# Kernel optimization log

Measured on AMD Instinct MI355X. Metric: run time of the kernel, lower is better.

## Reference

```python
import jax, jax.numpy as jnp
import numpy as np

N_NODES = 30000
N_REL = 8
N_EDGES = 150000
EMB = 128
HID = 128
OUT = 256
HEADS = 4
RANK = 8
SCALE = 1.0
NEG_SLOPE = 0.2
LN_EPS = 1e-5


def setup_inputs():
    key = jax.random.key(0)
    ks = jax.random.split(key, 16)
    def nrm(k, shp, s=0.05):
        return jax.random.normal(k, shp, dtype=jnp.float32) * s
    d2 = HEADS * HID  # conv2 input dim = 512
    return {
        "entity_emb": nrm(ks[0], (N_NODES, EMB)),
        "A1": nrm(ks[1], (N_REL, EMB * RANK)),
        "B1": nrm(ks[2], (N_REL, EMB * RANK)),
        "W1": nrm(ks[3], (HEADS * HID, EMB)),
        "att_l1": nrm(ks[4], (1, HEADS, HID)),
        "att_r1": nrm(ks[5], (1, HEADS, HID)),
        "relb1": jnp.zeros((N_REL, HEADS), jnp.float32),
        "bias1": jnp.zeros((HEADS * HID,), jnp.float32),
        "A2": nrm(ks[6], (N_REL, d2 * RANK)),
        "B2": nrm(ks[7], (N_REL, d2 * RANK)),
        "W2": nrm(ks[8], (OUT, d2)),
        "att_l2": nrm(ks[9], (1, 1, OUT)),
        "att_r2": nrm(ks[10], (1, 1, OUT)),
        "relb2": jnp.zeros((N_REL, 1), jnp.float32),
        "bias2": jnp.zeros((OUT,), jnp.float32),
        "res_W": nrm(ks[11], (OUT, EMB)),
        "res_b": jnp.zeros((OUT,), jnp.float32),
        "ln_g": jnp.ones((OUT,), jnp.float32),
        "ln_b": jnp.zeros((OUT,), jnp.float32),
        "edge_index": jax.random.randint(ks[12], (2, N_EDGES), 0, N_NODES),
        "edge_type": jax.random.randint(ks[13], (N_EDGES,), 0, N_REL),
    }


def _rel_gat_conv(x, A, B, W, att_l, att_r, relb, bias, j_idx, i_idx, etype, heads, out_dim, concat):
    # x: [N,d]; A,B: [R, d*k]; W: [heads*out_dim, d]
    N, d = x.shape
    R = A.shape[0]
    k = RANK
    HC = heads * out_dim
    A3 = A.reshape(R, d, k)
    B3 = B.reshape(R, d, k)
    z_all = x @ W.T  # [N, HC] base linear (shared by z_i and z_j)
    # LoRA low-rank projection per (node, relation): P[n,r] = B_r^T x_n
    P = jnp.einsum('nd,rdk->nrk', x, B3)          # [N,R,k] (small)
    low = P[j_idx, etype]                          # [E,k]
    # Fused LoRA-through-lin: lin(scale*A_r B_r^T x) = scale * low @ (A_r^T W^T)
    M = jnp.einsum('rdk,hd->rkh', A3, W).reshape(R * k, HC)  # [R*k, HC]
    oh = jax.nn.one_hot(etype, R, dtype=x.dtype)   # [E,R]
    low_exp = (oh[:, :, None] * low[:, None, :]).reshape(-1, R * k)  # [E,R*k]
    z_j = (z_all[j_idx] + SCALE * (low_exp @ M)).reshape(-1, heads, out_dim)  # [E,H,C]
    z_i = z_all[i_idx].reshape(-1, heads, out_dim)                            # [E,H,C]
    alpha = (z_i * att_l).sum(-1) + (z_j * att_r).sum(-1) + relb[etype]       # [E,H]
    alpha = jax.nn.leaky_relu(alpha, NEG_SLOPE)
    # per-relation loop => softmax groups are (relation, target node)
    seg = etype * N + i_idx
    n_seg = R * N
    amax = jax.ops.segment_max(alpha, seg, num_segments=n_seg)
    ex = jnp.exp(alpha - amax[seg])
    den = jax.ops.segment_sum(ex, seg, num_segments=n_seg)
    alpha = ex / den[seg]
    msg = z_j * alpha[:, :, None]                  # [E,H,C]
    out = jax.ops.segment_sum(msg, i_idx, num_segments=N)  # [N,H,C]
    out = out.reshape(N, HC) if concat else out.mean(axis=1)
    return out + bias


def _forward(entity_emb, A1, B1, W1, att_l1, att_r1, relb1, bias1,
             A2, B2, W2, att_l2, att_r2, relb2, bias2,
             res_W, res_b, ln_g, ln_b, edge_index, edge_type):
    j_idx, i_idx = edge_index[0], edge_index[1]
    x0 = entity_emb
    x = _rel_gat_conv(x0, A1, B1, W1, att_l1, att_r1, relb1, bias1,
                      j_idx, i_idx, edge_type, HEADS, HID, True)
    x = jax.nn.elu(x)
    x = _rel_gat_conv(x, A2, B2, W2, att_l2, att_r2, relb2, bias2,
                      j_idx, i_idx, edge_type, 1, OUT, False)
    x = x + (x0 @ res_W.T + res_b)
    mu = x.mean(axis=-1, keepdims=True)
    var = ((x - mu) ** 2).mean(axis=-1, keepdims=True)
    return (x - mu) / jnp.sqrt(var + LN_EPS) * ln_g + ln_b


def reference(entity_emb, A1, B1, W1, att_l1, att_r1, relb1, bias1,
              A2, B2, W2, att_l2, att_r2, relb2, bias2,
              res_W, res_b, ln_g, ln_b, edge_index, edge_type):
    return _forward(entity_emb, A1, B1, W1, att_l1, att_r1, relb1, bias1,
                    A2, B2, W2, att_l2, att_r2, relb2, bias2,
                    res_W, res_b, ln_g, ln_b, edge_index, edge_type)
```

## Files before the change

### kernel.cpp

```cpp
#include <hip/hip_runtime.h>
#include <cstddef>

#define NRELS 8
#define EMB 128
#define HID 128
#define OUTD 256
#define HEADS 4
#define RANK 8
#define D2 512
#define KCAT 192
#define NEG_SLOPE 0.2f
#define LN_EPS 1e-5f

typedef short bf16x8 __attribute__((ext_vector_type(8)));
typedef float f32x4 __attribute__((ext_vector_type(4)));

__device__ __forceinline__ unsigned short f2bf(float f) {
  union { float f; unsigned u; } v; v.f = f;
  unsigned u = v.u;
  return (unsigned short)((u + 0x7fffu + ((u >> 16) & 1u)) >> 16);
}
__device__ __forceinline__ float bf2f(unsigned short u) {
  union { unsigned u; float f; } v; v.u = (unsigned)u << 16; return v.f;
}

template<int ATT, int BIAS>
__global__ __launch_bounds__(256) void gemm_big_h(const unsigned short* __restrict__ A,
    const unsigned short* __restrict__ B, unsigned short* __restrict__ C, int M, int N, int K,
    const float* __restrict__ bias, const float* __restrict__ attL,
    const float* __restrict__ attR, float* __restrict__ al, float* __restrict__ ar) {
  __shared__ unsigned short As[128][36];
  __shared__ unsigned short Bs[128][36];
  __shared__ float pL[2][128];
  __shared__ float pR[2][128];
  const int tid = threadIdx.x;
  const int wave = tid >> 6;
  const int lane = tid & 63;
  const int wm = wave & 1;
  const int wn = wave >> 1;
  const int r16 = lane & 15;
  const int quad = lane >> 4;
  const int bm = blockIdx.x * 128;
  const int bn = blockIdx.y * 128;
  const int srow = tid >> 2;
  const int scol = (tid & 3) * 8;
  int ar0 = bm + srow;      if (ar0 >= M) ar0 = M - 1;
  int ar1 = bm + 64 + srow; if (ar1 >= M) ar1 = M - 1;
  const unsigned short* Ag0 = A + (size_t)ar0 * K + scol;
  const unsigned short* Ag1 = A + (size_t)ar1 * K + scol;
  const unsigned short* Bg0 = B + (size_t)(bn + srow) * K + scol;
  const unsigned short* Bg1 = B + (size_t)(bn + 64 + srow) * K + scol;
  f32x4 acc[4][4] = {};
  for (int k0 = 0; k0 < K; k0 += 32) {
    bf16x8 a0 = *(const bf16x8*)(Ag0 + k0);
    bf16x8 a1 = *(const bf16x8*)(Ag1 + k0);
    bf16x8 b0 = *(const bf16x8*)(Bg0 + k0);
    bf16x8 b1 = *(const bf16x8*)(Bg1 + k0);
    __syncthreads();
    *(bf16x8*)(&As[srow][scol]) = a0;
    *(bf16x8*)(&As[64 + srow][scol]) = a1;
    *(bf16x8*)(&Bs[srow][scol]) = b0;
    *(bf16x8*)(&Bs[64 + srow][scol]) = b1;
    __syncthreads();
    bf16x8 af[4], bfr[4];
#pragma unroll
    for (int mi = 0; mi < 4; ++mi)
      af[mi] = *(const bf16x8*)(&As[wm * 64 + mi * 16 + r16][quad * 8]);
#pragma unroll
    for (int ni = 0; ni < 4; ++ni)
      bfr[ni] = *(const bf16x8*)(&Bs[wn * 64 + ni * 16 + r16][quad * 8]);
#pragma unroll
    for (int mi = 0; mi < 4; ++mi)
#pragma unroll
      for (int ni = 0; ni < 4; ++ni)
        acc[mi][ni] = __builtin_amdgcn_mfma_f32_16x16x32_bf16(af[mi], bfr[ni], acc[mi][ni], 0, 0, 0);
  }
  float bcol[4];
  if (BIAS) {
#pragma unroll
    for (int ni = 0; ni < 4; ++ni) bcol[ni] = bias[bn + wn * 64 + ni * 16 + r16];
  }
#pragma unroll
  for (int mi = 0; mi < 4; ++mi)
#pragma unroll
    for (int ni = 0; ni < 4; ++ni)
#pragma unroll
      for (int r = 0; r < 4; ++r) {
        int row = bm + wm * 64 + mi * 16 + quad * 4 + r;
        if (row < M) {
          float v = acc[mi][ni][r];
          if (BIAS) v += bcol[ni];
          C[(size_t)row * N + bn + wn * 64 + ni * 16 + r16] = f2bf(v);
        }
      }
  if (ATT) {
    float La[4], Ra[4];
#pragma unroll
    for (int ni = 0; ni < 4; ++ni) {
      int cn = bn + wn * 64 + ni * 16 + r16;
      La[ni] = attL[cn]; Ra[ni] = attR[cn];
    }
#pragma unroll
    for (int mi = 0; mi < 4; ++mi)
#pragma unroll
      for (int r = 0; r < 4; ++r) {
        float sl = 0.f, sr = 0.f;
#pragma unroll
        for (int ni = 0; ni < 4; ++ni) {
          sl = fmaf(acc[mi][ni][r], La[ni], sl);
          sr = fmaf(acc[mi][ni][r], Ra[ni], sr);
        }
#pragma unroll
        for (int o = 1; o < 16; o <<= 1) {
          sl += __shfl_xor(sl, o, 64);
          sr += __shfl_xor(sr, o, 64);
        }
        if (r16 == 0) {
          int rl = wm * 64 + mi * 16 + quad * 4 + r;
          pL[wn][rl] = sl; pR[wn][rl] = sr;
        }
      }
    __syncthreads();
    if (tid < 128) {
      int row = bm + tid;
      if (row < M) {
        float sl = pL[0][tid] + pL[1][tid];
        float sr = pR[0][tid] + pR[1][tid];
        if (ATT == 1) {
          al[(size_t)row * 4 + blockIdx.y] = sl;
          ar[(size_t)row * 4 + blockIdx.y] = sr;
        } else {
          atomicAdd(&al[row], sl);
          atomicAdd(&ar[row], sr);
        }
      }
    }
  }
}

__global__ __launch_bounds__(256) void gemm_big(const unsigned short* __restrict__ A,
    const unsigned short* __restrict__ B, float* __restrict__ C, int M, int N, int K,
    const float* __restrict__ b0p, const float* __restrict__ b1p) {
  __shared__ unsigned short As[128][36];
  __shared__ unsigned short Bs[128][36];
  const int tid = threadIdx.x;
  const int wave = tid >> 6;
  const int lane = tid & 63;
  const int wm = wave & 1;
  const int wn = wave >> 1;
  const int r16 = lane & 15;
  const int quad = lane >> 4;
  const int bm = blockIdx.x * 128;
  const int bn = blockIdx.y * 128;
  const int srow = tid >> 2;
  const int scol = (tid & 3) * 8;
  int ar0 = bm + srow;      if (ar0 >= M) ar0 = M - 1;
  int ar1 = bm + 64 + srow; if (ar1 >= M) ar1 = M - 1;
  const unsigned short* Ag0 = A + (size_t)ar0 * K + scol;
  const unsigned short* Ag1 = A + (size_t)ar1 * K + scol;
  const unsigned short* Bg0 = B + (size_t)(bn + srow) * K + scol;
  const unsigned short* Bg1 = B + (size_t)(bn + 64 + srow) * K + scol;
  f32x4 acc[4][4] = {};
  for (int k0 = 0; k0 < K; k0 += 32) {
    bf16x8 a0 = *(const bf16x8*)(Ag0 + k0);
    bf16x8 a1 = *(const bf16x8*)(Ag1 + k0);
    bf16x8 b0 = *(const bf16x8*)(Bg0 + k0);
    bf16x8 b1 = *(const bf16x8*)(Bg1 + k0);
    __syncthreads();
    *(bf16x8*)(&As[srow][scol]) = a0;
    *(bf16x8*)(&As[64 + srow][scol]) = a1;
    *(bf16x8*)(&Bs[srow][scol]) = b0;
    *(bf16x8*)(&Bs[64 + srow][scol]) = b1;
    __syncthreads();
    bf16x8 af[4], bfr[4];
#pragma unroll
    for (int mi = 0; mi < 4; ++mi)
      af[mi] = *(const bf16x8*)(&As[wm * 64 + mi * 16 + r16][quad * 8]);
#pragma unroll
    for (int ni = 0; ni < 4; ++ni)
      bfr[ni] = *(const bf16x8*)(&Bs[wn * 64 + ni * 16 + r16][quad * 8]);
#pragma unroll
    for (int mi = 0; mi < 4; ++mi)
#pragma unroll
      for (int ni = 0; ni < 4; ++ni)
        acc[mi][ni] = __builtin_amdgcn_mfma_f32_16x16x32_bf16(af[mi], bfr[ni], acc[mi][ni], 0, 0, 0);
  }
  float badd[4];
#pragma unroll
  for (int ni = 0; ni < 4; ++ni) {
    int cn = bn + wn * 64 + ni * 16 + r16;
    badd[ni] = b0p[cn] + b1p[cn];
  }
#pragma unroll
  for (int mi = 0; mi < 4; ++mi)
#pragma unroll
    for (int ni = 0; ni < 4; ++ni)
#pragma unroll
      for (int r = 0; r < 4; ++r) {
        int row = bm + wm * 64 + mi * 16 + quad * 4 + r;
        if (row < M)
          C[(size_t)row * N + bn + wn * 64 + ni * 16 + r16] = acc[mi][ni][r] + badd[ni];
      }
}

__global__ __launch_bounds__(256) void gemm_bf16t(const unsigned short* __restrict__ A,
    const unsigned short* __restrict__ B, float* __restrict__ C, int M, int N, int K) {
  __shared__ unsigned short As[64][40];
  __shared__ unsigned short Bs[64][40];
  const int tid = threadIdx.x;
  const int wave = tid >> 6;
  const int lane = tid & 63;
  const int wm = wave & 1;
  const int wn = wave >> 1;
  const int r16 = lane & 15;
  const int quad = lane >> 4;
  const int bm = blockIdx.x * 64;
  const int bn = blockIdx.y * 64;
  const int srow = tid >> 2;
  const int schunk = tid & 3;
  int arow = bm + srow; if (arow >= M) arow = M - 1;
  const unsigned short* Ag = A + (size_t)arow * K + schunk * 8;
  const unsigned short* Bg = B + (size_t)(bn + srow) * K + schunk * 8;
  f32x4 acc[2][2] = {};
  for (int k0 = 0; k0 < K; k0 += 32) {
    bf16x8 av = *(const bf16x8*)(Ag + k0);
    bf16x8 bv = *(const bf16x8*)(Bg + k0);
    __syncthreads();
    *(bf16x8*)(&As[srow][schunk * 8]) = av;
    *(bf16x8*)(&Bs[srow][schunk * 8]) = bv;
    __syncthreads();
    bf16x8 af0 = *(const bf16x8*)(&As[wm * 32 + r16][quad * 8]);
    bf16x8 af1 = *(const bf16x8*)(&As[wm * 32 + 16 + r16][quad * 8]);
    bf16x8 bf0 = *(const bf16x8*)(&Bs[wn * 32 + r16][quad * 8]);
    bf16x8 bf1 = *(const bf16x8*)(&Bs[wn * 32 + 16 + r16][quad * 8]);
    acc[0][0] = __builtin_amdgcn_mfma_f32_16x16x32_bf16(af0, bf0, acc[0][0], 0, 0, 0);
    acc[0][1] = __builtin_amdgcn_mfma_f32_16x16x32_bf16(af0, bf1, acc[0][1], 0, 0, 0);
    acc[1][0] = __builtin_amdgcn_mfma_f32_16x16x32_bf16(af1, bf0, acc[1][0], 0, 0, 0);
    acc[1][1] = __builtin_amdgcn_mfma_f32_16x16x32_bf16(af1, bf1, acc[1][1], 0, 0, 0);
  }
#pragma unroll
  for (int mi = 0; mi < 2; ++mi)
#pragma unroll
    for (int ni = 0; ni < 2; ++ni)
#pragma unroll
      for (int r = 0; r < 4; ++r) {
        int row = bm + wm * 32 + mi * 16 + quad * 4 + r;
        if (row < M)
          C[(size_t)row * N + bn + wn * 32 + ni * 16 + r16] = acc[mi][ni][r];
      }
}

__global__ __launch_bounds__(256) void gemm_abt(const float* __restrict__ A,
    const float* __restrict__ B, float* __restrict__ C, int M, int N, int K) {
  __shared__ float As[32][64];
  __shared__ float Bs[32][64];
  const int tid = threadIdx.x;
  const int bm = blockIdx.y * 64;
  const int bn = blockIdx.x * 64;
  const int tx = tid & 15;
  const int ty = tid >> 4;
  const int lr = tid & 63;
  const int lq = tid >> 6;
  float acc[4][4] = {};
  for (int k0 = 0; k0 < K; k0 += 32) {
#pragma unroll
    for (int s = 0; s < 2; ++s) {
      const int q = lq + s * 4;
      const int gm = bm + lr;
      float4 va = make_float4(0.f, 0.f, 0.f, 0.f);
      if (gm < M) va = *(const float4*)(A + (size_t)gm * K + k0 + q * 4);
      As[q * 4 + 0][lr] = va.x; As[q * 4 + 1][lr] = va.y;
      As[q * 4 + 2][lr] = va.z; As[q * 4 + 3][lr] = va.w;
      const int gn = bn + lr;
      float4 vb = *(const float4*)(B + (size_t)gn * K + k0 + q * 4);
      Bs[q * 4 + 0][lr] = vb.x; Bs[q * 4 + 1][lr] = vb.y;
      Bs[q * 4 + 2][lr] = vb.z; Bs[q * 4 + 3][lr] = vb.w;
    }
    __syncthreads();
#pragma unroll
    for (int kk = 0; kk < 32; ++kk) {
      float a[4], b[4];
#pragma unroll
      for (int i2 = 0; i2 < 4; ++i2) { a[i2] = As[kk][ty * 4 + i2]; b[i2] = Bs[kk][tx * 4 + i2]; }
#pragma unroll
      for (int i2 = 0; i2 < 4; ++i2)
#pragma unroll
        for (int j2 = 0; j2 < 4; ++j2)
          acc[i2][j2] = fmaf(a[i2], b[j2], acc[i2][j2]);
    }
    __syncthreads();
  }
#pragma unroll
  for (int i2 = 0; i2 < 4; ++i2) {
    const int gm = bm + ty * 4 + i2;
    if (gm >= M) continue;
#pragma unroll
    for (int j2 = 0; j2 < 4; ++j2)
      C[(size_t)gm * N + bn + tx * 4 + j2] = acc[i2][j2];
  }
}

__global__ void prep_all(const float* __restrict__ x0, const float* __restrict__ W1,
    const float* __restrict__ W2, const float* __restrict__ res_W,
    const float* __restrict__ A1, const float* __restrict__ A2,
    const float* __restrict__ B1, const float* __restrict__ B2,
    unsigned short* __restrict__ x0b, unsigned short* __restrict__ Acat,
    unsigned short* __restrict__ W1b, unsigned short* __restrict__ W2b,
    unsigned short* __restrict__ RWcat,
    float* __restrict__ Amat1, float* __restrict__ Amat2,
    unsigned short* __restrict__ Bmat1b, unsigned short* __restrict__ Bmat2b, int nx0) {
  int idx = blockIdx.x * 256 + threadIdx.x;
  if (idx < nx0) { unsigned short b = f2bf(x0[idx]); x0b[idx] = b;
    Acat[(size_t)(idx >> 7) * KCAT + (idx & 127)] = b; return; } idx -= nx0;
  if (idx < D2 * EMB) { W1b[idx] = f2bf(W1[idx]); return; } idx -= D2 * EMB;
  if (idx < OUTD * D2) { W2b[idx] = f2bf(W2[idx]); return; } idx -= OUTD * D2;
  if (idx < OUTD * EMB) { RWcat[(size_t)(idx >> 7) * KCAT + (idx & 127)] = f2bf(res_W[idx]); return; } idx -= OUTD * EMB;
  if (idx < 64 * EMB) { int d = idx % EMB, rk = idx / EMB, k = rk & 7, r = rk >> 3;
    Amat1[idx] = A1[(size_t)r * EMB * RANK + (size_t)d * RANK + k]; return; } idx -= 64 * EMB;
  if (idx < 64 * D2) { int d = idx % D2, rk = idx / D2, k = rk & 7, r = rk >> 3;
    Amat2[idx] = A2[(size_t)r * D2 * RANK + (size_t)d * RANK + k]; return; } idx -= 64 * D2;
  if (idx < 64 * EMB) { int d = idx % EMB, rk = idx / EMB, k = rk & 7, r = rk >> 3;
    Bmat1b[idx] = f2bf(B1[(size_t)r * EMB * RANK + (size_t)d * RANK + k]); return; } idx -= 64 * EMB;
  if (idx < 64 * D2) { int d = idx % D2, rk = idx / D2, k = rk & 7, r = rk >> 3;
    Bmat2b[idx] = f2bf(B2[(size_t)r * D2 * RANK + (size_t)d * RANK + k]); }
}

__global__ void fold_att(const float* __restrict__ M1, const float* __restrict__ attR1,
                         const float* __restrict__ M2, const float* __restrict__ attR2,
                         float* __restrict__ Matt1, float* __restrict__ Matt2) {
  int t = threadIdx.x;
  if (blockIdx.x == 0) {
    int h = t & 3, rk = t >> 2;
    float s = 0.f;
    for (int c = 0; c < HID; ++c)
      s = fmaf(M1[(size_t)rk * D2 + h * HID + c], attR1[h * HID + c], s);
    Matt1[rk * 4 + h] = s;
  } else if (t < 64) {
    float s = 0.f;
    for (int c = 0; c < OUTD; ++c) s = fmaf(M2[(size_t)t * OUTD + c], attR2[c], s);
    Matt2[t] = s;
  }
}

__global__ void build_MT(const float* __restrict__ M1, const float* __restrict__ M2,
                         unsigned short* __restrict__ M1T, unsigned short* __restrict__ RWcat) {
  int idx = blockIdx.x * 256 + threadIdx.x;
  if (idx < 512 * 256) {
    int c = idx >> 8, s = idx & 255;
    int h = s >> 6, rk = s & 63;
    float v = ((c >> 7) == h) ? M1[(size_t)rk * D2 + c] : 0.f;
    M1T[idx] = f2bf(v);
  } else {
    idx -= 512 * 256;
    if (idx < 256 * 64) {
      int c = idx >> 6, rk = idx & 63;
      RWcat[(size_t)c * KCAT + 128 + rk] = f2bf(M2[(size_t)rk * OUTD + c]);
    }
  }
}

__global__ void hist_kernel(const int* __restrict__ ii, int* __restrict__ deg, int E) {
  int e = blockIdx.x * blockDim.x + threadIdx.x;
  if (e < E) atomicAdd(&deg[ii[e]], 1);
}

__global__ __launch_bounds__(1024) void exscan_kernel(const int* __restrict__ deg,
                                                      int* __restrict__ rowstart, int n) {
  __shared__ int wsum[16];
  int t = threadIdx.x;
  int lane = t & 63, wid = t >> 6;
  int carry = 0;
  for (int base = 0; base < n; base += 4096) {
    int i0 = base + t * 4;
    int v0 = 0, v1 = 0, v2 = 0, v3 = 0;
    if (i0 + 3 < n) {
      int4 vv = *(const int4*)(deg + i0);
      v0 = vv.x; v1 = vv.y; v2 = vv.z; v3 = vv.w;
    } else {
      if (i0 < n) v0 = deg[i0];
      if (i0 + 1 < n) v1 = deg[i0 + 1];
      if (i0 + 2 < n) v2 = deg[i0 + 2];
      if (i0 + 3 < n) v3 = deg[i0 + 3];
    }
    int tot = v0 + v1 + v2 + v3;
    int x = tot;
#pragma unroll
    for (int o = 1; o < 64; o <<= 1) {
      int y = __shfl_up(x, o, 64);
      if (lane >= o) x += y;
    }
    if (lane == 63) wsum[wid] = x;
    __syncthreads();
    if (t == 0) {
      int s = carry;
      for (int w2 = 0; w2 < 16; ++w2) { int tmp = wsum[w2]; wsum[w2] = s; s += tmp; }
      carry = s;
    }
    __syncthreads();
    int ex0 = x - tot + wsum[wid];
    if (i0 + 3 < n) {
      int4 ov; ov.x = ex0; ov.y = ex0 + v0; ov.z = ex0 + v0 + v1; ov.w = ex0 + v0 + v1 + v2;
      *(int4*)(rowstart + i0) = ov;
    } else {
      if (i0 < n) rowstart[i0] = ex0;
      if (i0 + 1 < n) rowstart[i0 + 1] = ex0 + v0;
      if (i0 + 2 < n) rowstart[i0 + 2] = ex0 + v0 + v1;
      if (i0 + 3 < n) rowstart[i0 + 3] = ex0 + v0 + v1 + v2;
    }
    __syncthreads();
  }
  if (t == 0) rowstart[n] = carry;
}

__global__ void scatter_kernel(const int* __restrict__ ii, const int* __restrict__ rowstart,
                               int* __restrict__ cursor, int* __restrict__ slot_of, int E) {
  int e = blockIdx.x * blockDim.x + threadIdx.x;
  if (e >= E) return;
  int i = ii[e];
  int p = atomicAdd(&cursor[i], 1);
  slot_of[e] = rowstart[i] + p;
}

__global__ void edge_alpha1(const int* __restrict__ ji, const int* __restrict__ ii,
                            const int* __restrict__ et, const int* __restrict__ slot_of,
                            const float* __restrict__ P1,
                            const float* __restrict__ al1, const float* __restrict__ ar1,
                            const float* __restrict__ relb1, const float* __restrict__ Matt1,
                            float4* __restrict__ recs1, int E) {
  int e = blockIdx.x * blockDim.x + threadIdx.x;
  if (e >= E) return;
  int j = ji[e], i = ii[e], rt = et[e];
  float4 lo0 = *(const float4*)(P1 + (size_t)j * 64 + rt * 8);
  float4 lo1 = *(const float4*)(P1 + (size_t)j * 64 + rt * 8 + 4);
  float low[RANK] = {lo0.x, lo0.y, lo0.z, lo0.w, lo1.x, lo1.y, lo1.z, lo1.w};
  float4 ali = *(const float4*)(al1 + (size_t)i * 4);
  float4 arj = *(const float4*)(ar1 + (size_t)j * 4);
  float4 rb  = *(const float4*)(relb1 + rt * 4);
  float a0 = ali.x + arj.x + rb.x;
  float a1 = ali.y + arj.y + rb.y;
  float a2 = ali.z + arj.z + rb.z;
  float a3 = ali.w + arj.w + rb.w;
#pragma unroll
  for (int k = 0; k < RANK; ++k) {
    float4 mk = *(const float4*)(Matt1 + ((rt * 8 + k) << 2));
    a0 = fmaf(low[k], mk.x, a0); a1 = fmaf(low[k], mk.y, a1);
    a2 = fmaf(low[k], mk.z, a2); a3 = fmaf(low[k], mk.w, a3);
  }
  a0 = (a0 > 0.f) ? a0 : NEG_SLOPE * a0;
  a1 = (a1 > 0.f) ? a1 : NEG_SLOPE * a1;
  a2 = (a2 > 0.f) ? a2 : NEG_SLOPE * a2;
  a3 = (a3 > 0.f) ? a3 : NEG_SLOPE * a3;
  float e0 = expf(a0), e1 = expf(a1), e2 = expf(a2), e3 = expf(a3);
  float4* rp = recs1 + (size_t)slot_of[e] * 4;
  rp[0] = make_float4(__int_as_float(j), e0, e1, e2);
  rp[1] = make_float4(e3, __int_as_float(rt), low[0], low[1]);
  rp[2] = make_float4(low[2], low[3], low[4], low[5]);
  rp[3] = make_float4(low[6], low[7], 0.f, 0.f);
}

__global__ __launch_bounds__(256) void qden1(float4* __restrict__ recs1,
    const int* __restrict__ rowstart, unsigned short* __restrict__ Q1b, int Nn) {
  __shared__ float denS[4][32];
  const int wid = threadIdx.x >> 6, lane = threadIdx.x & 63;
  const int i = blockIdx.x * 4 + wid;
  if (i >= Nn) return;
  const int rt_mine = lane >> 3, k = lane & 7;
  const int s0 = rowstart[i], deg = rowstart[i + 1] - s0;
  const float* rf = (const float*)recs1;
  float q0 = 0.f, q1 = 0.f, q2 = 0.f, q3 = 0.f;
  float d0 = 0.f, d1 = 0.f, d2 = 0.f, d3 = 0.f;
  float4 a0 = {}, a1 = {};
  float lw = 0.f;
  if (deg > 0) {
    a0 = recs1[(size_t)s0 * 4]; a1 = recs1[(size_t)s0 * 4 + 1];
    lw = rf[(size_t)s0 * 16 + 6 + k];
  }
  for (int p = 0; p < deg; ++p) {
    float4 b0 = a0, b1 = a1; float lwn = lw;
    if (p + 1 < deg) {
      b0 = recs1[(size_t)(s0 + p + 1) * 4]; b1 = recs1[(size_t)(s0 + p + 1) * 4 + 1];
      lwn = rf[(size_t)(s0 + p + 1) * 16 + 6 + k];
    }
    int rt = __float_as_int(a1.y);
    if (rt == rt_mine) {
      q0 = fmaf(a0.y, lw, q0); q1 = fmaf(a0.z, lw, q1);
      q2 = fmaf(a0.w, lw, q2); q3 = fmaf(a1.x, lw, q3);
      d0 += a0.y; d1 += a0.z; d2 += a0.w; d3 += a1.x;
    }
    a0 = b0; a1 = b1; lw = lwn;
  }
  float r0 = (d0 > 0.f) ? 1.f / d0 : 0.f;
  float r1 = (d1 > 0.f) ? 1.f / d1 : 0.f;
  float r2 = (d2 > 0.f) ? 1.f / d2 : 0.f;
  float r3 = (d3 > 0.f) ? 1.f / d3 : 0.f;
  size_t qb = (size_t)i * 256;
  Q1b[qb + lane]       = f2bf(q0 * r0);
  Q1b[qb + 64 + lane]  = f2bf(q1 * r1);
  Q1b[qb + 128 + lane] = f2bf(q2 * r2);
  Q1b[qb + 192 + lane] = f2bf(q3 * r3);
  if (k == 0) {
    denS[wid][rt_mine]      = r0;
    denS[wid][8 + rt_mine]  = r1;
    denS[wid][16 + rt_mine] = r2;
    denS[wid][24 + rt_mine] = r3;
  }
  for (int p = lane; p < deg; p += 64) {
    float4* rp = recs1 + (size_t)(s0 + p) * 4;
    float4 v0 = rp[0]; float4 v1 = rp[1];
    int rt = __float_as_int(v1.y);
    v0.y *= denS[wid][rt];      v0.z *= denS[wid][8 + rt];
    v0.w *= denS[wid][16 + rt]; v1.x *= denS[wid][24 + rt];
    rp[0] = v0; rp[1] = v1;
  }
}

__global__ __launch_bounds__(256) void node_agg1_lite(const float4* __restrict__ recs1,
    const int* __restrict__ rowstart, const unsigned short* __restrict__ z1b,
    const unsigned short* __restrict__ L1b, unsigned short* __restrict__ h1out, int Nn) {
  const int wid = threadIdx.x >> 6;
  const int lane = threadIdx.x & 63;
  const int i = blockIdx.x * 4 + wid;
  if (i >= Nn) return;
  const int s0 = rowstart[i];
  const int deg = rowstart[i + 1] - s0;
  const int c0 = lane * 8;
  const float* rf = (const float*)recs1;
  float acc[8] = {};
  float4 rc = {}, rn = {};
  float w3c = 0.f, w3n = 0.f;
  uint4 zc = {};
  if (deg > 0) {
    rc = recs1[(size_t)s0 * 4];
    w3c = rf[(size_t)s0 * 16 + 4];
    zc = *(const uint4*)(z1b + (size_t)__float_as_int(rc.x) * D2 + c0);
  }
  if (deg > 1) {
    rn = recs1[(size_t)(s0 + 1) * 4];
    w3n = rf[(size_t)(s0 + 1) * 16 + 4];
  }
  for (int p = 0; p < deg; ++p) {
    float4 r2 = rn; float w32 = w3n;
    uint4 zn = zc;
    if (p + 2 < deg) {
      r2 = recs1[(size_t)(s0 + p + 2) * 4];
      w32 = rf[(size_t)(s0 + p + 2) * 16 + 4];
    }
    if (p + 1 < deg)
      zn = *(const uint4*)(z1b + (size_t)__float_as_int(rn.x) * D2 + c0);
    float wlo = (lane & 16) ? rc.z : rc.y;
    float whi = (lane & 16) ? w3c : rc.w;
    float wt = (lane & 32) ? whi : wlo;
    acc[0] = fmaf(wt, bf2f((unsigned short)(zc.x & 0xffff)), acc[0]);
    acc[1] = fmaf(wt, bf2f((unsigned short)(zc.x >> 16)), acc[1]);
    acc[2] = fmaf(wt, bf2f((unsigned short)(zc.y & 0xffff)), acc[2]);
    acc[3] = fmaf(wt, bf2f((unsigned short)(zc.y >> 16)), acc[3]);
    acc[4] = fmaf(wt, bf2f((unsigned short)(zc.z & 0xffff)), acc[4]);
    acc[5] = fmaf(wt, bf2f((unsigned short)(zc.z >> 16)), acc[5]);
    acc[6] = fmaf(wt, bf2f((unsigned short)(zc.w & 0xffff)), acc[6]);
    acc[7] = fmaf(wt, bf2f((unsigned short)(zc.w >> 16)), acc[7]);
    rc = rn; w3c = w3n; rn = r2; w3n = w32; zc = zn;
  }
  uint4 lv = *(const uint4*)(L1b + (size_t)i * D2 + c0);
  unsigned lw[4] = {lv.x, lv.y, lv.z, lv.w};
  unsigned ov[4];
#pragma unroll
  for (int q = 0; q < 4; ++q) {
    float e0 = acc[2 * q]     + bf2f((unsigned short)(lw[q] & 0xffff));
    float e1 = acc[2 * q + 1] + bf2f((unsigned short)(lw[q] >> 16));
    e0 = e0 > 0.f ? e0 : expm1f(e0);
    e1 = e1 > 0.f ? e1 : expm1f(e1);
    ov[q] = (unsigned)f2bf(e0) | ((unsigned)f2bf(e1) << 16);
  }
  *(uint4*)(h1out + (size_t)i * D2 + c0) = make_uint4(ov[0], ov[1], ov[2], ov[3]);
}

__global__ void edge_alpha2(const int* __restrict__ ji, const int* __restrict__ ii,
                            const int* __restrict__ et, const int* __restrict__ slot_of,
                            const float* __restrict__ P2,
                            const float* __restrict__ al2, const float* __restrict__ ar2,
                            const float* __restrict__ relb2, const float* __restrict__ Matt2,
                            float4* __restrict__ recs2, int E) {
  int e = blockIdx.x * blockDim.x + threadIdx.x;
  if (e >= E) return;
  int j = ji[e], i = ii[e], rt = et[e];
  float4 lo0 = *(const float4*)(P2 + (size_t)j * 64 + rt * 8);
  float4 lo1 = *(const float4*)(P2 + (size_t)j * 64 + rt * 8 + 4);
  float low[RANK] = {lo0.x, lo0.y, lo0.z, lo0.w, lo1.x, lo1.y, lo1.z, lo1.w};
  float a = al2[i] + ar2[j] + relb2[rt];
#pragma unroll
  for (int k = 0; k < RANK; ++k) a = fmaf(low[k], Matt2[rt * RANK + k], a);
  a = (a > 0.f) ? a : NEG_SLOPE * a;
  float ex = expf(a);
  float4* rp = recs2 + (size_t)slot_of[e] * 3;
  rp[0] = make_float4(__int_as_float(j), __int_as_float(rt), ex, low[0]);
  rp[1] = make_float4(low[1], low[2], low[3], low[4]);
  rp[2] = make_float4(low[5], low[6], low[7], 0.f);
}

__global__ __launch_bounds__(256) void qden2(float4* __restrict__ recs2,
    const int* __restrict__ rowstart, unsigned short* __restrict__ Acat, int Nn) {
  __shared__ float denS[4][NRELS];
  const int wid = threadIdx.x >> 6, lane = threadIdx.x & 63;
  const int i = blockIdx.x * 4 + wid;
  if (i >= Nn) return;
  const int rt_mine = lane >> 3, k = lane & 7;
  const int s0 = rowstart[i], deg = rowstart[i + 1] - s0;
  const float* rf = (const float*)recs2;
  float q = 0.f, d = 0.f;
  float4 a0 = {}; float lw = 0.f;
  if (deg > 0) { a0 = recs2[(size_t)s0 * 3]; lw = rf[(size_t)s0 * 12 + 3 + k]; }
  for (int p = 0; p < deg; ++p) {
    float4 b0 = a0; float lwn = lw;
    if (p + 1 < deg) {
      b0 = recs2[(size_t)(s0 + p + 1) * 3];
      lwn = rf[(size_t)(s0 + p + 1) * 12 + 3 + k];
    }
    int rt = __float_as_int(a0.y);
    if (rt == rt_mine) { q = fmaf(a0.z, lw, q); d += a0.z; }
    a0 = b0; lw = lwn;
  }
  float rd = (d > 0.f) ? 1.f / d : 0.f;
  Acat[(size_t)i * KCAT + 128 + lane] = f2bf(q * rd);
  if (k == 0) denS[wid][rt_mine] = rd;
  for (int p = lane; p < deg; p += 64) {
    float* ep = (float*)(recs2 + (size_t)(s0 + p) * 3);
    int rt = __float_as_int(ep[1]);
    ep[2] *= denS[wid][rt];
  }
}

__global__ __launch_bounds__(256) void node_agg2_lite(const float4* __restrict__ recs2,
    const int* __restrict__ rowstart, const unsigned short* __restrict__ z2b,
    const float* __restrict__ o2, const float* __restrict__ ln_g,
    const float* __restrict__ ln_b, float* __restrict__ y, int Nn) {
  const int wid = threadIdx.x >> 6;
  const int lane = threadIdx.x & 63;
  const int i = blockIdx.x * 4 + wid;
  if (i >= Nn) return;
  const int s0 = rowstart[i];
  const int deg = rowstart[i + 1] - s0;
  const int c0 = lane * 4;
  float acc[4] = {};
  float4 rc = {}, rn = {};
  uint2 zc = make_uint2(0u, 0u);
  if (deg > 0) {
    rc = recs2[(size_t)s0 * 3];
    zc = *(const uint2*)(z2b + (size_t)__float_as_int(rc.x) * OUTD + c0);
  }
  if (deg > 1) rn = recs2[(size_t)(s0 + 1) * 3];
  for (int p = 0; p < deg; ++p) {
    float4 r2 = rn;
    uint2 zn = zc;
    if (p + 2 < deg) r2 = recs2[(size_t)(s0 + p + 2) * 3];
    if (p + 1 < deg)
      zn = *(const uint2*)(z2b + (size_t)__float_as_int(rn.x) * OUTD + c0);
    float wt = rc.z;
    acc[0] = fmaf(wt, bf2f((unsigned short)(zc.x & 0xffff)), acc[0]);
    acc[1] = fmaf(wt, bf2f((unsigned short)(zc.x >> 16)), acc[1]);
    acc[2] = fmaf(wt, bf2f((unsigned short)(zc.y & 0xffff)), acc[2]);
    acc[3] = fmaf(wt, bf2f((unsigned short)(zc.y >> 16)), acc[3]);
    rc = rn; rn = r2; zc = zn;
  }
  float4 rsv = *(const float4*)(o2 + (size_t)i * OUTD + c0);
  float vv[4];
  vv[0] = acc[0] + rsv.x;
  vv[1] = acc[1] + rsv.y;
  vv[2] = acc[2] + rsv.z;
  vv[3] = acc[3] + rsv.w;
  float s = vv[0] + vv[1] + vv[2] + vv[3];
  for (int o = 32; o > 0; o >>= 1) s += __shfl_xor(s, o, 64);
  float mu = s * (1.f / OUTD);
  float q = 0.f;
#pragma unroll
  for (int k = 0; k < 4; ++k) { float d = vv[k] - mu; q += d * d; }
  for (int o = 32; o > 0; o >>= 1) q += __shfl_xor(q, o, 64);
  float rstd = rsqrtf(q * (1.f / OUTD) + LN_EPS);
  float4 g = *(const float4*)(ln_g + c0);
  float4 bb = *(const float4*)(ln_b + c0);
  float4 ov;
  ov.x = (vv[0] - mu) * rstd * g.x + bb.x;
  ov.y = (vv[1] - mu) * rstd * g.y + bb.y;
  ov.z = (vv[2] - mu) * rstd * g.z + bb.z;
  ov.w = (vv[3] - mu) * rstd * g.w + bb.w;
  *(float4*)(y + (size_t)i * OUTD + c0) = ov;
}

extern "C" void kernel_launch(void* const* d_in, const int* in_sizes, int n_in,
                              void* d_out, int out_size, void* d_ws, size_t ws_size,
                              hipStream_t stream) {
  const float* x0     = (const float*)d_in[0];
  const float* A1     = (const float*)d_in[1];
  const float* B1     = (const float*)d_in[2];
  const float* W1     = (const float*)d_in[3];
  const float* attL1  = (const float*)d_in[4];
  const float* attR1  = (const float*)d_in[5];
  const float* relb1  = (const float*)d_in[6];
  const float* bias1  = (const float*)d_in[7];
  const float* A2     = (const float*)d_in[8];
  const float* B2     = (const float*)d_in[9];
  const float* W2     = (const float*)d_in[10];
  const float* attL2  = (const float*)d_in[11];
  const float* attR2  = (const float*)d_in[12];
  const float* relb2  = (const float*)d_in[13];
  const float* bias2  = (const float*)d_in[14];
  const float* res_W  = (const float*)d_in[15];
  const float* res_b  = (const float*)d_in[16];
  const float* ln_g   = (const float*)d_in[17];
  const float* ln_b   = (const float*)d_in[18];
  const int*   eidx   = (const int*)d_in[19];
  const int*   etype  = (const int*)d_in[20];
  float* out = (float*)d_out;

  const int Nn = in_sizes[0] / EMB;
  const int E  = in_sizes[20];
  const int* ji = eidx;
  const int* ii = eidx + E;

  float* w = (float*)d_ws;
  size_t off = 0;
  float* o2    = w + off; off += (size_t)Nn * OUTD;
  float* P1    = w + off; off += (size_t)Nn * 64;
  float* P2    = w + off; off += (size_t)Nn * 64;
  float* M1    = w + off; off += 64 * D2;
  float* M2    = w + off; off += 64 * OUTD;
  float* Amat1 = w + off; off += 64 * EMB;
  float* Amat2 = w + off; off += 64 * D2;
  float* Matt1 = w + off; off += 64 * 4;
  float* Matt2 = w + off; off += 64;
  float* al1   = w + off; off += (size_t)Nn * 4;
  float* ar1   = w + off; off += (size_t)Nn * 4;
  float* al2   = w + off; off += (size_t)Nn;
  float* ar2   = w + off; off += (size_t)Nn;
  float4* recs1 = (float4*)(w + off); off += (size_t)E * 16;
  float4* recs2 = (float4*)(w + off); off += (size_t)E * 12;
  unsigned short* z1b    = (unsigned short*)(w + off); off += (size_t)Nn * D2 / 2;
  unsigned short* z2b    = (unsigned short*)(w + off); off += (size_t)Nn * OUTD / 2;
  unsigned short* x0b    = (unsigned short*)(w + off); off += (size_t)Nn * EMB / 2;
  unsigned short* h1b    = (unsigned short*)(w + off); off += (size_t)Nn * D2 / 2;
  unsigned short* W1b    = (unsigned short*)(w + off); off += (size_t)D2 * EMB / 2;
  unsigned short* W2b    = (unsigned short*)(w + off); off += (size_t)OUTD * D2 / 2;
  unsigned short* Bmat1b = (unsigned short*)(w + off); off += (size_t)64 * EMB / 2;
  unsigned short* Bmat2b = (unsigned short*)(w + off); off += (size_t)64 * D2 / 2;
  unsigned short* Acat   = (unsigned short*)(w + off); off += (size_t)Nn * KCAT / 2;
  unsigned short* RWcat  = (unsigned short*)(w + off); off += (size_t)OUTD * KCAT / 2;
  unsigned short* M1T    = (unsigned short*)(w + off); off += (size_t)512 * 256 / 2;
  int* ideg     = (int*)(w + off); off += (size_t)Nn;
  int* cursor   = (int*)(w + off); off += (size_t)Nn;
  int* slot_of  = (int*)(w + off); off += (size_t)E;
  int* rowstart = (int*)(w + off); off += (size_t)Nn + 1;
  (void)ws_size; (void)n_in; (void)out_size;

  unsigned short* Q1b = (unsigned short*)P1;
  unsigned short* L1b = (unsigned short*)o2;

  const int MT64 = (Nn + 63) / 64;
  const int MT128 = (Nn + 127) / 128;
  const int NB4 = (Nn + 3) / 4;

  (void)hipMemsetAsync(ideg, 0, (size_t)Nn * sizeof(int), stream);
  (void)hipMemsetAsync(cursor, 0, (size_t)Nn * sizeof(int), stream);
  (void)hipMemsetAsync(al2, 0, (size_t)Nn * sizeof(float), stream);
  (void)hipMemsetAsync(ar2, 0, (size_t)Nn * sizeof(float), stream);
  hist_kernel<<<(E + 255) / 256, 256, 0, stream>>>(ii, ideg, E);
  exscan_kernel<<<1, 1024, 0, stream>>>(ideg, rowstart, Nn);
  scatter_kernel<<<(E + 255) / 256, 256, 0, stream>>>(ii, rowstart, cursor, slot_of, E);

  {
    int nx0 = Nn * EMB;
    int total = nx0 + D2 * EMB + OUTD * D2 + OUTD * EMB + 64 * EMB + 64 * D2 + 64 * EMB + 64 * D2;
    prep_all<<<(total + 255) / 256, 256, 0, stream>>>(x0, W1, W2, res_W, A1, A2, B1, B2,
        x0b, Acat, W1b, W2b, RWcat, Amat1, Amat2, Bmat1b, Bmat2b, nx0);
  }

  gemm_abt<<<dim3(D2 / 64, 1), 256, 0, stream>>>(Amat1, W1, M1, 64, D2, EMB);
  gemm_abt<<<dim3(OUTD / 64, 1), 256, 0, stream>>>(Amat2, W2, M2, 64, OUTD, D2);
  fold_att<<<2, 256, 0, stream>>>(M1, attR1, M2, attR2, Matt1, Matt2);
  build_MT<<<(512 * 256 + 256 * 64 + 255) / 256, 256, 0, stream>>>(M1, M2, M1T, RWcat);

  gemm_big_h<1, 0><<<dim3(MT128, D2 / 128), 256, 0, stream>>>(x0b, W1b, z1b, Nn, D2, EMB,
      nullptr, attL1, attR1, al1, ar1);
  gemm_bf16t<<<dim3(MT64, 1), 256, 0, stream>>>(x0b, Bmat1b, P1, Nn, 64, EMB);

  edge_alpha1<<<(E + 255) / 256, 256, 0, stream>>>(ji, ii, etype, slot_of, P1, al1, ar1,
                                                   relb1, Matt1, recs1, E);
  qden1<<<NB4, 256, 0, stream>>>(recs1, rowstart, Q1b, Nn);
  gemm_big_h<0, 1><<<dim3(MT128, D2 / 128), 256, 0, stream>>>(Q1b, M1T, L1b, Nn, D2, 256,
      bias1, nullptr, nullptr, nullptr, nullptr);
  node_agg1_lite<<<NB4, 256, 0, stream>>>(recs1, rowstart, z1b, L1b, h1b, Nn);

  gemm_big_h<2, 0><<<dim3(MT128, OUTD / 128), 256, 0, stream>>>(h1b, W2b, z2b, Nn, OUTD, D2,
      nullptr, attL2, attR2, al2, ar2);
  gemm_bf16t<<<dim3(MT64, 1), 256, 0, stream>>>(h1b, Bmat2b, P2, Nn, 64, D2);

  edge_alpha2<<<(E + 255) / 256, 256, 0, stream>>>(ji, ii, etype, slot_of, P2, al2, ar2,
                                                   relb2, Matt2, recs2, E);
  qden2<<<NB4, 256, 0, stream>>>(recs2, rowstart, Acat, Nn);
  gemm_big<<<dim3(MT128, OUTD / 128), 256, 0, stream>>>(Acat, RWcat, o2, Nn, OUTD, KCAT,
      bias2, res_b);
  node_agg2_lite<<<NB4, 256, 0, stream>>>(recs2, rowstart, z2b, o2, ln_g, ln_b, out, Nn);
}
```

Measured before the change: 415.8 us.

## Use direct global-to-LDS loads with swizzle in GEMMs and drop CSR scatter pass

The GEMM tiles now load with global_load_lds straight into an XOR-swizzled LDS layout, which removes the register round trip and the padded shared arrays. The f32-output GEMM is folded into the same template. The histogram kernel now records each edge's position within its destination row, so the separate scatter kernel and the cursor memset go away. The atomic accumulation of layer-2 attention logits is replaced by per-column-block partial buffers that edge_alpha2 sums, which also removes two memsets. The risks are ordering and swizzle correctness of the async LDS loads, plus an extra read per edge.

```diff
diff --git a/kernel.cpp b/kernel.cpp
--- a/kernel.cpp
+++ b/kernel.cpp
@@ -24,13 +24,19 @@
   union { unsigned u; float f; } v; v.u = (unsigned)u << 16; return v.f;
 }
 
-template<int ATT, int BIAS>
-__global__ __launch_bounds__(256) void gemm_big_h(const unsigned short* __restrict__ A,
-    const unsigned short* __restrict__ B, unsigned short* __restrict__ C, int M, int N, int K,
-    const float* __restrict__ bias, const float* __restrict__ attL,
-    const float* __restrict__ attR, float* __restrict__ al, float* __restrict__ ar) {
-  __shared__ unsigned short As[128][36];
-  __shared__ unsigned short Bs[128][36];
+#define GLOAD16(ldsp, gp) \
+  __builtin_amdgcn_global_load_lds((const __attribute__((address_space(1))) unsigned int*)(gp), \
+      (__attribute__((address_space(3))) unsigned int*)(ldsp), 16, 0, 0)
+
+template<int ATT, int BIAS, int F32OUT>
+__global__ __launch_bounds__(256) void gemm_tile(const unsigned short* __restrict__ A,
+    const unsigned short* __restrict__ B, unsigned short* __restrict__ C,
+    float* __restrict__ Cf, int M, int N, int K,
+    const float* __restrict__ bias, const float* __restrict__ b1p,
+    const float* __restrict__ attL, const float* __restrict__ attR,
+    float* __restrict__ al, float* __restrict__ ar) {
+  __shared__ unsigned short As[128 * 32];
+  __shared__ unsigned short Bs[128 * 32];
   __shared__ float pL[2][128];
   __shared__ float pR[2][128];
   const int tid = threadIdx.x;
@@ -42,33 +48,34 @@
   const int quad = lane >> 4;
   const int bm = blockIdx.x * 128;
   const int bn = blockIdx.y * 128;
-  const int srow = tid >> 2;
-  const int scol = (tid & 3) * 8;
-  int ar0 = bm + srow;      if (ar0 >= M) ar0 = M - 1;
-  int ar1 = bm + 64 + srow; if (ar1 >= M) ar1 = M - 1;
-  const unsigned short* Ag0 = A + (size_t)ar0 * K + scol;
-  const unsigned short* Ag1 = A + (size_t)ar1 * K + scol;
-  const unsigned short* Bg0 = B + (size_t)(bn + srow) * K + scol;
-  const unsigned short* Bg1 = B + (size_t)(bn + 64 + srow) * K + scol;
+  const int lr = lane >> 2;
+  const int lc = (((lane & 3) ^ ((lane >> 3) & 3))) * 8;
+  int arow0 = bm + wave * 32 + lr;      if (arow0 >= M) arow0 = M - 1;
+  int arow1 = bm + wave * 32 + 16 + lr; if (arow1 >= M) arow1 = M - 1;
+  const unsigned short* Ag0 = A + (size_t)arow0 * K + lc;
+  const unsigned short* Ag1 = A + (size_t)arow1 * K + lc;
+  const unsigned short* Bg0 = B + (size_t)(bn + wave * 32 + lr) * K + lc;
+  const unsigned short* Bg1 = B + (size_t)(bn + wave * 32 + 16 + lr) * K + lc;
+  unsigned short* lA0 = As + wave * 1024;
+  unsigned short* lA1 = As + wave * 1024 + 512;
+  unsigned short* lB0 = Bs + wave * 1024;
+  unsigned short* lB1 = Bs + wave * 1024 + 512;
+  const int rsw = (quad ^ ((r16 >> 1) & 3)) * 8;
   f32x4 acc[4][4] = {};
   for (int k0 = 0; k0 < K; k0 += 32) {
-    bf16x8 a0 = *(const bf16x8*)(Ag0 + k0);
-    bf16x8 a1 = *(const bf16x8*)(Ag1 + k0);
-    bf16x8 b0 = *(const bf16x8*)(Bg0 + k0);
-    bf16x8 b1 = *(const bf16x8*)(Bg1 + k0);
-    __syncthreads();
-    *(bf16x8*)(&As[srow][scol]) = a0;
-    *(bf16x8*)(&As[64 + srow][scol]) = a1;
-    *(bf16x8*)(&Bs[srow][scol]) = b0;
-    *(bf16x8*)(&Bs[64 + srow][scol]) = b1;
+    __syncthreads();
+    GLOAD16(lA0, Ag0 + k0);
+    GLOAD16(lA1, Ag1 + k0);
+    GLOAD16(lB0, Bg0 + k0);
+    GLOAD16(lB1, Bg1 + k0);
     __syncthreads();
     bf16x8 af[4], bfr[4];
 #pragma unroll
     for (int mi = 0; mi < 4; ++mi)
-      af[mi] = *(const bf16x8*)(&As[wm * 64 + mi * 16 + r16][quad * 8]);
+      af[mi] = *(const bf16x8*)(As + (wm * 64 + mi * 16 + r16) * 32 + rsw);
 #pragma unroll
     for (int ni = 0; ni < 4; ++ni)
-      bfr[ni] = *(const bf16x8*)(&Bs[wn * 64 + ni * 16 + r16][quad * 8]);
+      bfr[ni] = *(const bf16x8*)(Bs + (wn * 64 + ni * 16 + r16) * 32 + rsw);
 #pragma unroll
     for (int mi = 0; mi < 4; ++mi)
 #pragma unroll
@@ -78,7 +85,11 @@
   float bcol[4];
   if (BIAS) {
 #pragma unroll
-    for (int ni = 0; ni < 4; ++ni) bcol[ni] = bias[bn + wn * 64 + ni * 16 + r16];
+    for (int ni = 0; ni < 4; ++ni) {
+      int cn = bn + wn * 64 + ni * 16 + r16;
+      bcol[ni] = bias[cn];
+      if (F32OUT) bcol[ni] += b1p[cn];
+    }
   }
 #pragma unroll
   for (int mi = 0; mi < 4; ++mi)
@@ -90,7 +101,9 @@
         if (row < M) {
           float v = acc[mi][ni][r];
           if (BIAS) v += bcol[ni];
-          C[(size_t)row * N + bn + wn * 64 + ni * 16 + r16] = f2bf(v);
+          size_t idx = (size_t)row * N + bn + wn * 64 + ni * 16 + r16;
+          if (F32OUT) Cf[idx] = v;
+          else        C[idx] = f2bf(v);
         }
       }
   if (ATT) {
@@ -130,77 +143,12 @@
           al[(size_t)row * 4 + blockIdx.y] = sl;
           ar[(size_t)row * 4 + blockIdx.y] = sr;
         } else {
-          atomicAdd(&al[row], sl);
-          atomicAdd(&ar[row], sr);
+          al[(size_t)blockIdx.y * M + row] = sl;
+          ar[(size_t)blockIdx.y * M + row] = sr;
         }
       }
     }
   }
-}
-
-__global__ __launch_bounds__(256) void gemm_big(const unsigned short* __restrict__ A,
-    const unsigned short* __restrict__ B, float* __restrict__ C, int M, int N, int K,
-    const float* __restrict__ b0p, const float* __restrict__ b1p) {
-  __shared__ unsigned short As[128][36];
-  __shared__ unsigned short Bs[128][36];
-  const int tid = threadIdx.x;
-  const int wave = tid >> 6;
-  const int lane = tid & 63;
-  const int wm = wave & 1;
-  const int wn = wave >> 1;
-  const int r16 = lane & 15;
-  const int quad = lane >> 4;
-  const int bm = blockIdx.x * 128;
-  const int bn = blockIdx.y * 128;
-  const int srow = tid >> 2;
-  const int scol = (tid & 3) * 8;
-  int ar0 = bm + srow;      if (ar0 >= M) ar0 = M - 1;
-  int ar1 = bm + 64 + srow; if (ar1 >= M) ar1 = M - 1;
-  const unsigned short* Ag0 = A + (size_t)ar0 * K + scol;
-  const unsigned short* Ag1 = A + (size_t)ar1 * K + scol;
-  const unsigned short* Bg0 = B + (size_t)(bn + srow) * K + scol;
-  const unsigned short* Bg1 = B + (size_t)(bn + 64 + srow) * K + scol;
-  f32x4 acc[4][4] = {};
-  for (int k0 = 0; k0 < K; k0 += 32) {
-    bf16x8 a0 = *(const bf16x8*)(Ag0 + k0);
-    bf16x8 a1 = *(const bf16x8*)(Ag1 + k0);
-    bf16x8 b0 = *(const bf16x8*)(Bg0 + k0);
-    bf16x8 b1 = *(const bf16x8*)(Bg1 + k0);
-    __syncthreads();
-    *(bf16x8*)(&As[srow][scol]) = a0;
-    *(bf16x8*)(&As[64 + srow][scol]) = a1;
-    *(bf16x8*)(&Bs[srow][scol]) = b0;
-    *(bf16x8*)(&Bs[64 + srow][scol]) = b1;
-    __syncthreads();
-    bf16x8 af[4], bfr[4];
-#pragma unroll
-    for (int mi = 0; mi < 4; ++mi)
-      af[mi] = *(const bf16x8*)(&As[wm * 64 + mi * 16 + r16][quad * 8]);
-#pragma unroll
-    for (int ni = 0; ni < 4; ++ni)
-      bfr[ni] = *(const bf16x8*)(&Bs[wn * 64 + ni * 16 + r16][quad * 8]);
-#pragma unroll
-    for (int mi = 0; mi < 4; ++mi)
-#pragma unroll
-      for (int ni = 0; ni < 4; ++ni)
-        acc[mi][ni] = __builtin_amdgcn_mfma_f32_16x16x32_bf16(af[mi], bfr[ni], acc[mi][ni], 0, 0, 0);
-  }
-  float badd[4];
-#pragma unroll
-  for (int ni = 0; ni < 4; ++ni) {
-    int cn = bn + wn * 64 + ni * 16 + r16;
-    badd[ni] = b0p[cn] + b1p[cn];
-  }
-#pragma unroll
-  for (int mi = 0; mi < 4; ++mi)
-#pragma unroll
-    for (int ni = 0; ni < 4; ++ni)
-#pragma unroll
-      for (int r = 0; r < 4; ++r) {
-        int row = bm + wm * 64 + mi * 16 + quad * 4 + r;
-        if (row < M)
-          C[(size_t)row * N + bn + wn * 64 + ni * 16 + r16] = acc[mi][ni][r] + badd[ni];
-      }
 }
 
 __global__ __launch_bounds__(256) void gemm_bf16t(const unsigned short* __restrict__ A,
@@ -359,9 +307,10 @@
   }
 }
 
-__global__ void hist_kernel(const int* __restrict__ ii, int* __restrict__ deg, int E) {
+__global__ void hist_kernel(const int* __restrict__ ii, int* __restrict__ deg,
+                            int* __restrict__ prepos, int E) {
   int e = blockIdx.x * blockDim.x + threadIdx.x;
-  if (e < E) atomicAdd(&deg[ii[e]], 1);
+  if (e < E) prepos[e] = atomicAdd(&deg[ii[e]], 1);
 }
 
 __global__ __launch_bounds__(1024) void exscan_kernel(const int* __restrict__ deg,
@@ -412,17 +361,9 @@
   if (t == 0) rowstart[n] = carry;
 }
 
-__global__ void scatter_kernel(const int* __restrict__ ii, const int* __restrict__ rowstart,
-                               int* __restrict__ cursor, int* __restrict__ slot_of, int E) {
-  int e = blockIdx.x * blockDim.x + threadIdx.x;
-  if (e >= E) return;
-  int i = ii[e];
-  int p = atomicAdd(&cursor[i], 1);
-  slot_of[e] = rowstart[i] + p;
-}
-
 __global__ void edge_alpha1(const int* __restrict__ ji, const int* __restrict__ ii,
-                            const int* __restrict__ et, const int* __restrict__ slot_of,
+                            const int* __restrict__ et, const int* __restrict__ rowstart,
+                            const int* __restrict__ prepos,
                             const float* __restrict__ P1,
                             const float* __restrict__ al1, const float* __restrict__ ar1,
                             const float* __restrict__ relb1, const float* __restrict__ Matt1,
@@ -451,7 +392,7 @@
   a2 = (a2 > 0.f) ? a2 : NEG_SLOPE * a2;
   a3 = (a3 > 0.f) ? a3 : NEG_SLOPE * a3;
   float e0 = expf(a0), e1 = expf(a1), e2 = expf(a2), e3 = expf(a3);
-  float4* rp = recs1 + (size_t)slot_of[e] * 4;
+  float4* rp = recs1 + (size_t)(rowstart[i] + prepos[e]) * 4;
   rp[0] = make_float4(__int_as_float(j), e0, e1, e2);
   rp[1] = make_float4(e3, __int_as_float(rt), low[0], low[1]);
   rp[2] = make_float4(low[2], low[3], low[4], low[5]);
@@ -575,23 +516,24 @@
 }
 
 __global__ void edge_alpha2(const int* __restrict__ ji, const int* __restrict__ ii,
-                            const int* __restrict__ et, const int* __restrict__ slot_of,
+                            const int* __restrict__ et, const int* __restrict__ rowstart,
+                            const int* __restrict__ prepos,
                             const float* __restrict__ P2,
                             const float* __restrict__ al2, const float* __restrict__ ar2,
                             const float* __restrict__ relb2, const float* __restrict__ Matt2,
-                            float4* __restrict__ recs2, int E) {
+                            float4* __restrict__ recs2, int E, int Nn) {
   int e = blockIdx.x * blockDim.x + threadIdx.x;
   if (e >= E) return;
   int j = ji[e], i = ii[e], rt = et[e];
   float4 lo0 = *(const float4*)(P2 + (size_t)j * 64 + rt * 8);
   float4 lo1 = *(const float4*)(P2 + (size_t)j * 64 + rt * 8 + 4);
   float low[RANK] = {lo0.x, lo0.y, lo0.z, lo0.w, lo1.x, lo1.y, lo1.z, lo1.w};
-  float a = al2[i] + ar2[j] + relb2[rt];
+  float a = al2[i] + al2[(size_t)Nn + i] + ar2[j] + ar2[(size_t)Nn + j] + relb2[rt];
 #pragma unroll
   for (int k = 0; k < RANK; ++k) a = fmaf(low[k], Matt2[rt * RANK + k], a);
   a = (a > 0.f) ? a : NEG_SLOPE * a;
   float ex = expf(a);
-  float4* rp = recs2 + (size_t)slot_of[e] * 3;
+  float4* rp = recs2 + (size_t)(rowstart[i] + prepos[e]) * 3;
   rp[0] = make_float4(__int_as_float(j), __int_as_float(rt), ex, low[0]);
   rp[1] = make_float4(low[1], low[2], low[3], low[4]);
   rp[2] = make_float4(low[5], low[6], low[7], 0.f);
@@ -729,8 +671,8 @@
   float* Matt2 = w + off; off += 64;
   float* al1   = w + off; off += (size_t)Nn * 4;
   float* ar1   = w + off; off += (size_t)Nn * 4;
-  float* al2   = w + off; off += (size_t)Nn;
-  float* ar2   = w + off; off += (size_t)Nn;
+  float* al2   = w + off; off += (size_t)Nn * 2;
+  float* ar2   = w + off; off += (size_t)Nn * 2;
   float4* recs1 = (float4*)(w + off); off += (size_t)E * 16;
   float4* recs2 = (float4*)(w + off); off += (size_t)E * 12;
   unsigned short* z1b    = (unsigned short*)(w + off); off += (size_t)Nn * D2 / 2;
@@ -745,8 +687,7 @@
   unsigned short* RWcat  = (unsigned short*)(w + off); off += (size_t)OUTD * KCAT / 2;
   unsigned short* M1T    = (unsigned short*)(w + off); off += (size_t)512 * 256 / 2;
   int* ideg     = (int*)(w + off); off += (size_t)Nn;
-  int* cursor   = (int*)(w + off); off += (size_t)Nn;
-  int* slot_of  = (int*)(w + off); off += (size_t)E;
+  int* prepos   = (int*)(w + off); off += (size_t)E;
   int* rowstart = (int*)(w + off); off += (size_t)Nn + 1;
   (void)ws_size; (void)n_in; (void)out_size;
 
@@ -758,12 +699,8 @@
   const int NB4 = (Nn + 3) / 4;
 
   (void)hipMemsetAsync(ideg, 0, (size_t)Nn * sizeof(int), stream);
-  (void)hipMemsetAsync(cursor, 0, (size_t)Nn * sizeof(int), stream);
-  (void)hipMemsetAsync(al2, 0, (size_t)Nn * sizeof(float), stream);
-  (void)hipMemsetAsync(ar2, 0, (size_t)Nn * sizeof(float), stream);
-  hist_kernel<<<(E + 255) / 256, 256, 0, stream>>>(ii, ideg, E);
+  hist_kernel<<<(E + 255) / 256, 256, 0, stream>>>(ii, ideg, prepos, E);
   exscan_kernel<<<1, 1024, 0, stream>>>(ideg, rowstart, Nn);
-  scatter_kernel<<<(E + 255) / 256, 256, 0, stream>>>(ii, rowstart, cursor, slot_of, E);
 
   {
     int nx0 = Nn * EMB;
@@ -777,25 +714,25 @@
   fold_att<<<2, 256, 0, stream>>>(M1, attR1, M2, attR2, Matt1, Matt2);
   build_MT<<<(512 * 256 + 256 * 64 + 255) / 256, 256, 0, stream>>>(M1, M2, M1T, RWcat);
 
-  gemm_big_h<1, 0><<<dim3(MT128, D2 / 128), 256, 0, stream>>>(x0b, W1b, z1b, Nn, D2, EMB,
-      nullptr, attL1, attR1, al1, ar1);
+  gemm_tile<1, 0, 0><<<dim3(MT128, D2 / 128), 256, 0, stream>>>(x0b, W1b, z1b, nullptr,
+      Nn, D2, EMB, nullptr, nullptr, attL1, attR1, al1, ar1);
   gemm_bf16t<<<dim3(MT64, 1), 256, 0, stream>>>(x0b, Bmat1b, P1, Nn, 64, EMB);
 
-  edge_alpha1<<<(E + 255) / 256, 256, 0, stream>>>(ji, ii, etype, slot_of, P1, al1, ar1,
-                                                   relb1, Matt1, recs1, E);
+  edge_alpha1<<<(E + 255) / 256, 256, 0, stream>>>(ji, ii, etype, rowstart, prepos, P1,
+                                                   al1, ar1, relb1, Matt1, recs1, E);
   qden1<<<NB4, 256, 0, stream>>>(recs1, rowstart, Q1b, Nn);
-  gemm_big_h<0, 1><<<dim3(MT128, D2 / 128), 256, 0, stream>>>(Q1b, M1T, L1b, Nn, D2, 256,
-      bias1, nullptr, nullptr, nullptr, nullptr);
+  gemm_tile<0, 1, 0><<<dim3(MT128, D2 / 128), 256, 0, stream>>>(Q1b, M1T, L1b, nullptr,
+      Nn, D2, 256, bias1, nullptr, nullptr, nullptr, nullptr, nullptr);
   node_agg1_lite<<<NB4, 256, 0, stream>>>(recs1, rowstart, z1b, L1b, h1b, Nn);
 
-  gemm_big_h<2, 0><<<dim3(MT128, OUTD / 128), 256, 0, stream>>>(h1b, W2b, z2b, Nn, OUTD, D2,
-      nullptr, attL2, attR2, al2, ar2);
+  gemm_tile<2, 0, 0><<<dim3(MT128, OUTD / 128), 256, 0, stream>>>(h1b, W2b, z2b, nullptr,
+      Nn, OUTD, D2, nullptr, nullptr, attL2, attR2, al2, ar2);
   gemm_bf16t<<<dim3(MT64, 1), 256, 0, stream>>>(h1b, Bmat2b, P2, Nn, 64, D2);
 
-  edge_alpha2<<<(E + 255) / 256, 256, 0, stream>>>(ji, ii, etype, slot_of, P2, al2, ar2,
-                                                   relb2, Matt2, recs2, E);
+  edge_alpha2<<<(E + 255) / 256, 256, 0, stream>>>(ji, ii, etype, rowstart, prepos, P2,
+                                                   al2, ar2, relb2, Matt2, recs2, E, Nn);
   qden2<<<NB4, 256, 0, stream>>>(recs2, rowstart, Acat, Nn);
-  gemm_big<<<dim3(MT128, OUTD / 128), 256, 0, stream>>>(Acat, RWcat, o2, Nn, OUTD, KCAT,
-      bias2, res_b);
+  gemm_tile<0, 1, 1><<<dim3(MT128, OUTD / 128), 256, 0, stream>>>(Acat, RWcat, nullptr, o2,
+      Nn, OUTD, KCAT, bias2, res_b, nullptr, nullptr, nullptr, nullptr);
   node_agg2_lite<<<NB4, 256, 0, stream>>>(recs2, rowstart, z2b, o2, ln_g, ln_b, out, Nn);
 }
```

New measurement: 401.9 us. 3.3% less time.
